# Performance work log

Measured on AMD Instinct MI355X. Metric: run time of the kernel, lower is better.

The kernel has to match this reference:

```python
import jax, jax.numpy as jnp
import numpy as np

H = 2048      # hidden_size
I = 8192      # intermediate_size
NH = 16       # num_heads
HD = H // NH  # head_dim
EPS = 1e-6


def setup_inputs() -> dict:
    key = jax.random.key(0)
    ks = jax.random.split(key, 10)
    s = 0.02
    return {
        "hidden_states": jax.random.normal(ks[0], (2, 2048, H), dtype=jnp.float32),
        "wq": jax.random.normal(ks[1], (H, H), dtype=jnp.float32) * s,
        "wk": jax.random.normal(ks[2], (H, H), dtype=jnp.float32) * s,
        "wv": jax.random.normal(ks[3], (H, H), dtype=jnp.float32) * s,
        "wo": jax.random.normal(ks[4], (H, H), dtype=jnp.float32) * s,
        "w_gate": jax.random.normal(ks[5], (H, I), dtype=jnp.float32) * s,
        "w_up": jax.random.normal(ks[6], (H, I), dtype=jnp.float32) * s,
        "w_down": jax.random.normal(ks[7], (I, H), dtype=jnp.float32) * s,
        "ln1_w": jnp.ones((H,), dtype=jnp.float32),
        "ln2_w": jnp.ones((H,), dtype=jnp.float32),
    }


def rmsnorm(x, w):
    xf = x.astype(jnp.float32)
    var = jnp.mean(xf * xf, axis=-1, keepdims=True)
    return w * (xf * jax.lax.rsqrt(var + EPS)).astype(x.dtype)


def reference(hidden_states, wq, wk, wv, wo, w_gate, w_up, w_down, ln1_w, ln2_w):
    b, s, _ = hidden_states.shape
    residual = hidden_states
    x = rmsnorm(hidden_states, ln1_w)

    # attention (no RoPE, no causal mask, per source)
    q = (x @ wq).reshape(b, s, NH, HD)
    k = (x @ wk).reshape(b, s, NH, HD)
    v = (x @ wv).reshape(b, s, NH, HD)
    scores = jnp.einsum('bqhd,bkhd->bhqk', q, k) / jnp.sqrt(jnp.float32(HD))
    attn = jax.nn.softmax(scores, axis=-1)
    out = jnp.einsum('bhqk,bkhd->bqhd', attn, v).reshape(b, s, H)
    hidden = residual + out @ wo

    residual = hidden
    y = rmsnorm(hidden, ln2_w)
    gate = jax.nn.silu(y @ w_gate)
    up = y @ w_up
    return residual + (gate * up) @ w_down
```

## Files before the change

### kernel.cpp

```cpp
#include <hip/hip_runtime.h>
#include <hip/hip_bf16.h>

#define HDIM 2048
#define IDIM 8192
#define NHEADS 16
#define HEADD 128
#define BATCH 2
#define SEQ 2048
#define MTOK 4096

typedef unsigned short u16;
typedef __bf16 bf16x8 __attribute__((ext_vector_type(8)));
typedef float f32x4 __attribute__((ext_vector_type(4)));
typedef float f32x16 __attribute__((ext_vector_type(16)));
typedef unsigned short u16x8 __attribute__((ext_vector_type(8)));
typedef unsigned int u32x2 __attribute__((ext_vector_type(2)));
typedef unsigned int u32x4 __attribute__((ext_vector_type(4)));
typedef unsigned int uv2 __attribute__((ext_vector_type(2)));

__device__ __forceinline__ u16 f2b(float f) {
  unsigned u = __builtin_bit_cast(unsigned, f);
  u += 0x7FFFu + ((u >> 16) & 1u);
  return (u16)(u >> 16);
}
__device__ __forceinline__ float b2f(u16 b) {
  unsigned u = ((unsigned)b) << 16;
  return __builtin_bit_cast(float, u);
}
__device__ __forceinline__ void gl_lds16(const void* g, void* l) {
  auto gp = (const __attribute__((address_space(1))) unsigned int*)((unsigned long long)g);
  auto lp = (__attribute__((address_space(3))) unsigned int*)((unsigned)(unsigned long long)l);
  __builtin_amdgcn_global_load_lds(gp, lp, 16, 0, 0);
}
__device__ __forceinline__ unsigned cvtpk(float lo, float hi) {
  unsigned r;
  asm("v_cvt_pk_bf16_f32 %0, %1, %2" : "=v"(r) : "v"(lo), "v"(hi));
  return r;
}

__global__ __launch_bounds__(256) void wtrans_all(const float* __restrict__ wq, const float* __restrict__ wk,
                                                  const float* __restrict__ wv, const float* __restrict__ wo,
                                                  const float* __restrict__ wg, const float* __restrict__ wu,
                                                  const float* __restrict__ wd,
                                                  u16* __restrict__ wqkvT, u16* __restrict__ woT,
                                                  u16* __restrict__ wgT, u16* __restrict__ wuT,
                                                  u16* __restrict__ wdT) {
  int bidf = blockIdx.x;
  const float* W;
  u16* Wt;
  int K, N, rowoff, bx, by;
  if (bidf < 3072) {
    int s = bidf >> 10, r = bidf & 1023;
    W = s == 0 ? wq : (s == 1 ? wk : wv);
    Wt = wqkvT; K = 2048; N = 2048; rowoff = s * 2048;
    bx = r & 31; by = r >> 5;
  } else if (bidf < 4096) {
    int r = bidf - 3072;
    W = wo; Wt = woT; K = 2048; N = 2048; rowoff = 0;
    bx = r & 31; by = r >> 5;
  } else if (bidf < 8192) {
    int r = bidf - 4096;
    W = wg; Wt = wgT; K = 2048; N = 8192; rowoff = 0;
    bx = r & 127; by = r >> 7;
  } else if (bidf < 12288) {
    int r = bidf - 8192;
    W = wu; Wt = wuT; K = 2048; N = 8192; rowoff = 0;
    bx = r & 127; by = r >> 7;
  } else {
    int r = bidf - 12288;
    W = wd; Wt = wdT; K = 8192; N = 2048; rowoff = 0;
    bx = r & 31; by = r >> 5;
  }
  __shared__ float t[64][65];
  int n0 = bx * 64, k0 = by * 64;
  int tid = threadIdx.x;
  int kr = tid >> 4, nc = (tid & 15) * 4;
#pragma unroll
  for (int p = 0; p < 4; p++) {
    float4 v = *(const float4*)&W[(size_t)(k0 + p * 16 + kr) * N + n0 + nc];
    t[nc + 0][p * 16 + kr] = v.x;
    t[nc + 1][p * 16 + kr] = v.y;
    t[nc + 2][p * 16 + kr] = v.z;
    t[nc + 3][p * 16 + kr] = v.w;
  }
  __syncthreads();
  int n = tid >> 2, kq = (tid & 3) * 16;
  u16 tmp[16];
#pragma unroll
  for (int i = 0; i < 16; i++) tmp[i] = f2b(t[n][kq + i]);
  *(u16x8*)&Wt[(size_t)(rowoff + n0 + n) * K + k0 + kq] = *(u16x8*)&tmp[0];
  *(u16x8*)&Wt[(size_t)(rowoff + n0 + n) * K + k0 + kq + 8] = *(u16x8*)&tmp[8];
}

__global__ __launch_bounds__(256) void vtrans_k(const u16* __restrict__ qkv, u16* __restrict__ vt) {
  __shared__ u16 t[32][33];
  int s0 = blockIdx.x * 32, d0 = blockIdx.y * 32, bh = blockIdx.z;
  int b = bh >> 4, h = bh & 15;
  int tx = threadIdx.x, ty = threadIdx.y;
#pragma unroll
  for (int i = 0; i < 4; i++)
    t[ty + i * 8][tx] = qkv[(size_t)(b * SEQ + s0 + ty + i * 8) * 6144 + 4096 + h * HEADD + d0 + tx];
  __syncthreads();
#pragma unroll
  for (int i = 0; i < 4; i++)
    vt[(size_t)(bh * HEADD + d0 + ty + i * 8) * SEQ + s0 + tx] = t[tx][ty + i * 8];
}

__global__ __launch_bounds__(256) void rmsnorm_k(const float* __restrict__ X, const float* __restrict__ W,
                                                 u16* __restrict__ O) {
  int row = blockIdx.x;
  int tid = threadIdx.x;
  const float* x = X + (size_t)row * HDIM;
  float4 v0 = ((const float4*)x)[tid * 2];
  float4 v1 = ((const float4*)x)[tid * 2 + 1];
  float ss = v0.x * v0.x + v0.y * v0.y + v0.z * v0.z + v0.w * v0.w
           + v1.x * v1.x + v1.y * v1.y + v1.z * v1.z + v1.w * v1.w;
#pragma unroll
  for (int off = 32; off > 0; off >>= 1) ss += __shfl_down(ss, off);
  __shared__ float red[4];
  if ((tid & 63) == 0) red[tid >> 6] = ss;
  __syncthreads();
  float rs = rsqrtf((red[0] + red[1] + red[2] + red[3]) * (1.0f / HDIM) + 1e-6f);
  const float* w = W + tid * 8;
  u16* o = O + (size_t)row * HDIM + tid * 8;
  float vals[8] = {v0.x, v0.y, v0.z, v0.w, v1.x, v1.y, v1.z, v1.w};
#pragma unroll
  for (int j = 0; j < 8; j++) o[j] = f2b(w[j] * vals[j] * rs);
}

__global__ __launch_bounds__(512, 2) void gemm_fgu(const u16* __restrict__ A, const u16* __restrict__ Bg,
                                                   const u16* __restrict__ Bu, u16* __restrict__ G) {
  __shared__ char lds[131072];
  const int tid = threadIdx.x, lane = tid & 63, w = tid >> 6;
  const int wm = w >> 2, wn = w & 3;
  const int bid = blockIdx.y * 64 + blockIdx.x;
  const int swz = (bid & 7) * 128 + (bid >> 3);
  const int bx = swz & 63, by = swz >> 6;
  const int m0 = by * 256, n0 = bx * 128;
  const int NT = 32;

  const int srow = w * 8 + (lane >> 3);
  const int kko = ((lane & 7) ^ (lane >> 3)) * 8;
  const u16* Asrc = A + (size_t)(m0 + srow) * 2048 + kko;
  const u16* Bgsrc = Bg + (size_t)(n0 + srow) * 2048 + kko;
  const u16* Busrc = Bu + (size_t)(n0 + srow) * 2048 + kko;
  const int wofs = w * 1024;

#define SA0(buf, kt)                                                        \
  {                                                                         \
    gl_lds16(Asrc + (kt) * 64, lds + (buf) * 65536 + wofs);                 \
    gl_lds16(Asrc + 64 * 2048 + (kt) * 64, lds + (buf) * 65536 + 8192 + wofs); \
  }
#define SA1(buf, kt)                                                              \
  {                                                                               \
    gl_lds16(Asrc + 128 * 2048 + (kt) * 64, lds + (buf) * 65536 + 16384 + wofs);  \
    gl_lds16(Asrc + 192 * 2048 + (kt) * 64, lds + (buf) * 65536 + 24576 + wofs);  \
  }
#define SBG(buf, kt)                                                              \
  {                                                                               \
    gl_lds16(Bgsrc + (kt) * 64, lds + (buf) * 65536 + 32768 + wofs);              \
    gl_lds16(Bgsrc + 64 * 2048 + (kt) * 64, lds + (buf) * 65536 + 40960 + wofs);  \
  }
#define SBU(buf, kt)                                                              \
  {                                                                               \
    gl_lds16(Busrc + (kt) * 64, lds + (buf) * 65536 + 49152 + wofs);              \
    gl_lds16(Busrc + 64 * 2048 + (kt) * 64, lds + (buf) * 65536 + 57344 + wofs);  \
  }
#define LG0 { asm volatile("s_waitcnt lgkmcnt(0)" ::: "memory"); __builtin_amdgcn_sched_barrier(0); }

  const int l15 = lane & 15, l4 = lane >> 4;
  const int kq0 = ((l4) ^ (l15 & 7)) << 4;
  const int kq1 = ((4 + l4) ^ (l15 & 7)) << 4;
  const int abase = (wm * 128 + l15) * 128;
  const int gbase = 32768 + (wn * 32 + l15) * 128;
  const int ubase = 49152 + (wn * 32 + l15) * 128;

  const f32x4 fz = {0.f, 0.f, 0.f, 0.f};
  f32x4 ag[8][2], au[8][2];
#pragma unroll
  for (int i = 0; i < 8; i++)
#pragma unroll
    for (int j = 0; j < 2; j++) { ag[i][j] = fz; au[i][j] = fz; }
  bf16x8 af[8], bgf[2], buf2[2];

  SA0(0, 0);
  SBG(0, 0);
  SA1(0, 0);
  SBU(0, 0);
  asm volatile("s_waitcnt vmcnt(2)" ::: "memory");
  __builtin_amdgcn_s_barrier();

  for (int t = 0; t < NT; ++t) {
    const int buf = t & 1, nb = buf ^ 1;
    const char* Lb = lds + buf * 65536;
    const int t1 = (t + 1 < NT) ? t + 1 : NT - 1;
#pragma unroll
    for (int mf = 0; mf < 8; mf++) af[mf] = *(const bf16x8*)(Lb + abase + mf * 2048 + kq0);
    bgf[0] = *(const bf16x8*)(Lb + gbase + kq0);
    bgf[1] = *(const bf16x8*)(Lb + gbase + 2048 + kq0);
    SA0(nb, t1);
    SBG(nb, t1);
    __builtin_amdgcn_s_barrier();
    LG0;
    __builtin_amdgcn_s_setprio(1);
#pragma unroll
    for (int mf = 0; mf < 8; mf++) {
      ag[mf][0] = __builtin_amdgcn_mfma_f32_16x16x32_bf16(af[mf], bgf[0], ag[mf][0], 0, 0, 0);
      ag[mf][1] = __builtin_amdgcn_mfma_f32_16x16x32_bf16(af[mf], bgf[1], ag[mf][1], 0, 0, 0);
    }
    __builtin_amdgcn_s_setprio(0);
    asm volatile("s_waitcnt vmcnt(4)" ::: "memory");
    __builtin_amdgcn_s_barrier();
    buf2[0] = *(const bf16x8*)(Lb + ubase + kq0);
    buf2[1] = *(const bf16x8*)(Lb + ubase + 2048 + kq0);
    SA1(nb, t1);
    __builtin_amdgcn_s_barrier();
    LG0;
    __builtin_amdgcn_s_setprio(1);
#pragma unroll
    for (int mf = 0; mf < 8; mf++) {
      au[mf][0] = __builtin_amdgcn_mfma_f32_16x16x32_bf16(af[mf], buf2[0], au[mf][0], 0, 0, 0);
      au[mf][1] = __builtin_amdgcn_mfma_f32_16x16x32_bf16(af[mf], buf2[1], au[mf][1], 0, 0, 0);
    }
    __builtin_amdgcn_s_setprio(0);
    __builtin_amdgcn_s_barrier();
#pragma unroll
    for (int mf = 0; mf < 8; mf++) af[mf] = *(const bf16x8*)(Lb + abase + mf * 2048 + kq1);
    bgf[0] = *(const bf16x8*)(Lb + gbase + kq1);
    bgf[1] = *(const bf16x8*)(Lb + gbase + 2048 + kq1);
    __builtin_amdgcn_s_barrier();
    LG0;
    __builtin_amdgcn_s_setprio(1);
#pragma unroll
    for (int mf = 0; mf < 8; mf++) {
      ag[mf][0] = __builtin_amdgcn_mfma_f32_16x16x32_bf16(af[mf], bgf[0], ag[mf][0], 0, 0, 0);
      ag[mf][1] = __builtin_amdgcn_mfma_f32_16x16x32_bf16(af[mf], bgf[1], ag[mf][1], 0, 0, 0);
    }
    __builtin_amdgcn_s_setprio(0);
    __builtin_amdgcn_s_barrier();
    buf2[0] = *(const bf16x8*)(Lb + ubase + kq1);
    buf2[1] = *(const bf16x8*)(Lb + ubase + 2048 + kq1);
    SBU(nb, t1);
    __builtin_amdgcn_s_barrier();
    LG0;
    __builtin_amdgcn_s_setprio(1);
#pragma unroll
    for (int mf = 0; mf < 8; mf++) {
      au[mf][0] = __builtin_amdgcn_mfma_f32_16x16x32_bf16(af[mf], buf2[0], au[mf][0], 0, 0, 0);
      au[mf][1] = __builtin_amdgcn_mfma_f32_16x16x32_bf16(af[mf], buf2[1], au[mf][1], 0, 0, 0);
    }
    __builtin_amdgcn_s_setprio(0);
    asm volatile("s_waitcnt vmcnt(2)" ::: "memory");
    __builtin_amdgcn_s_barrier();
  }
  asm volatile("s_waitcnt vmcnt(0)" ::: "memory");

#pragma unroll
  for (int mf = 0; mf < 8; mf++) {
#pragma unroll
    for (int jr = 0; jr < 4; jr++) {
      const int m = m0 + wm * 128 + mf * 16 + l4 * 4 + jr;
#pragma unroll
      for (int nf = 0; nf < 2; nf++) {
        const int n = n0 + wn * 32 + nf * 16 + l15;
        float g = ag[mf][nf][jr];
        float u = au[mf][nf][jr];
        float sg = g / (1.f + __expf(-g));
        G[(size_t)m * IDIM + n] = f2b(sg * u);
      }
    }
  }
#undef SA0
#undef SA1
#undef SBG
#undef SBU
#undef LG0
}

template <int EPI>
__global__ __launch_bounds__(512, 2) void gemm_w(const u16* __restrict__ A, const u16* __restrict__ Bt,
                                                 int M, int N, int K,
                                                 u16* __restrict__ Cb, float* __restrict__ Cf,
                                                 const float* __restrict__ Res, u16* __restrict__ Gm) {
  __shared__ char lds[131072];
  const int tid = threadIdx.x;
  const int lane = tid & 63, w = tid >> 6;
  const int wm = w >> 2, wn = w & 3;
  const int bid = blockIdx.y * gridDim.x + blockIdx.x;
  const int xcd = bid & 7, idx = bid >> 3;
  const int round = idx >> 4, j = idx & 15;
  const int nsy4 = gridDim.y >> 2;
  const int st = round * 8 + xcd;
  const int sx = st / nsy4, syi = st % nsy4;
  const int by = syi * 4 + (j & 3), bx = sx * 4 + (j >> 2);
  const int m0 = by * 256, n0 = bx * 256;
  const int NT = K >> 6;

  const int srow = w * 8 + (lane >> 3);
  const int kko = ((lane & 7) ^ (lane >> 3)) * 8;
  const u16* Asrc = A + (size_t)(m0 + srow) * K + kko;
  const u16* Bsrc = Bt + (size_t)(n0 + srow) * K + kko;
  const int wofs = w * 1024;

#define STAGE_AH(buf, kt, h)                                                          \
  {                                                                                   \
    gl_lds16(Asrc + ((size_t)((h) * 128) * K) + (size_t)(kt) * 64,                    \
             lds + (buf) * 65536 + (h) * 16384 + wofs);                               \
    gl_lds16(Asrc + ((size_t)((h) * 128 + 64) * K) + (size_t)(kt) * 64,               \
             lds + (buf) * 65536 + (h) * 16384 + 8192 + wofs);                        \
  }
#define STAGE_BH(buf, kt, h)                                                          \
  {                                                                                   \
    gl_lds16(Bsrc + ((size_t)((h) * 128) * K) + (size_t)(kt) * 64,                    \
             lds + (buf) * 65536 + 32768 + (h) * 16384 + wofs);                       \
    gl_lds16(Bsrc + ((size_t)((h) * 128 + 64) * K) + (size_t)(kt) * 64,               \
             lds + (buf) * 65536 + 32768 + (h) * 16384 + 8192 + wofs);                \
  }
#define LG0 { asm volatile("s_waitcnt lgkmcnt(0)" ::: "memory"); __builtin_amdgcn_sched_barrier(0); }

  const int l15 = lane & 15, l4 = lane >> 4;
  const int kq0 = ((l4) ^ (l15 & 7)) << 4;
  const int kq1 = ((4 + l4) ^ (l15 & 7)) << 4;
  const int abase = wm * 16384 + l15 * 128;
  const int bbase = 32768 + (wn >> 1) * 16384 + ((wn & 1) * 64 + l15) * 128;

  const f32x4 fz = {0.f, 0.f, 0.f, 0.f};
  f32x4 acc[8][4];
#pragma unroll
  for (int i = 0; i < 8; i++)
#pragma unroll
    for (int jj = 0; jj < 4; jj++) acc[i][jj] = fz;
  bf16x8 af[4], bfr[4];

  STAGE_AH(0, 0, 0);
  STAGE_AH(0, 0, 1);
  STAGE_BH(0, 0, 0);
  STAGE_BH(0, 0, 1);
  STAGE_AH(1, 1, 0);
  STAGE_BH(1, 1, 0);
  asm volatile("s_waitcnt vmcnt(4)" ::: "memory");
  __builtin_amdgcn_s_barrier();

  for (int t = 0; t < NT; ++t) {
    const int buf = t & 1, nbuf = buf ^ 1;
    const char* Lb = lds + buf * 65536;
    const int t1 = (t + 1 < NT) ? t + 1 : NT - 1;
    const int t2 = (t + 2 < NT) ? t + 2 : NT - 1;
#pragma unroll
    for (int mf = 0; mf < 4; mf++) af[mf] = *(const bf16x8*)(Lb + abase + mf * 2048 + kq0);
#pragma unroll
    for (int nf = 0; nf < 4; nf++) bfr[nf] = *(const bf16x8*)(Lb + bbase + nf * 2048 + kq0);
    STAGE_AH(nbuf, t1, 1);
    STAGE_BH(nbuf, t1, 1);
    __builtin_amdgcn_s_barrier();
    LG0;
    __builtin_amdgcn_s_setprio(1);
#pragma unroll
    for (int mf = 0; mf < 4; mf++)
#pragma unroll
      for (int nf = 0; nf < 4; nf++)
        acc[mf][nf] = __builtin_amdgcn_mfma_f32_16x16x32_bf16(af[mf], bfr[nf], acc[mf][nf], 0, 0, 0);
    __builtin_amdgcn_s_setprio(0);
    __builtin_amdgcn_s_barrier();
#pragma unroll
    for (int mf = 0; mf < 4; mf++) af[mf] = *(const bf16x8*)(Lb + abase + (mf + 4) * 2048 + kq0);
    __builtin_amdgcn_s_barrier();
    LG0;
    __builtin_amdgcn_s_setprio(1);
#pragma unroll
    for (int mf = 0; mf < 4; mf++)
#pragma unroll
      for (int nf = 0; nf < 4; nf++)
        acc[mf + 4][nf] = __builtin_amdgcn_mfma_f32_16x16x32_bf16(af[mf], bfr[nf], acc[mf + 4][nf], 0, 0, 0);
    __builtin_amdgcn_s_setprio(0);
    __builtin_amdgcn_s_barrier();
#pragma unroll
    for (int mf = 0; mf < 4; mf++) af[mf] = *(const bf16x8*)(Lb + abase + mf * 2048 + kq1);
#pragma unroll
    for (int nf = 0; nf < 4; nf++) bfr[nf] = *(const bf16x8*)(Lb + bbase + nf * 2048 + kq1);
    __builtin_amdgcn_s_barrier();
    LG0;
    __builtin_amdgcn_s_setprio(1);
#pragma unroll
    for (int mf = 0; mf < 4; mf++)
#pragma unroll
      for (int nf = 0; nf < 4; nf++)
        acc[mf][nf] = __builtin_amdgcn_mfma_f32_16x16x32_bf16(af[mf], bfr[nf], acc[mf][nf], 0, 0, 0);
    __builtin_amdgcn_s_setprio(0);
    __builtin_amdgcn_s_barrier();
#pragma unroll
    for (int mf = 0; mf < 4; mf++) af[mf] = *(const bf16x8*)(Lb + abase + (mf + 4) * 2048 + kq1);
    STAGE_AH(buf, t2, 0);
    STAGE_BH(buf, t2, 0);
    __builtin_amdgcn_s_barrier();
    LG0;
    __builtin_amdgcn_s_setprio(1);
#pragma unroll
    for (int mf = 0; mf < 4; mf++)
#pragma unroll
      for (int nf = 0; nf < 4; nf++)
        acc[mf + 4][nf] = __builtin_amdgcn_mfma_f32_16x16x32_bf16(af[mf], bfr[nf], acc[mf + 4][nf], 0, 0, 0);
    __builtin_amdgcn_s_setprio(0);
    asm volatile("s_waitcnt vmcnt(4)" ::: "memory");
    __builtin_amdgcn_s_barrier();
  }
  asm volatile("s_waitcnt vmcnt(0)" ::: "memory");

  const int r0 = l4 * 4;
#pragma unroll
  for (int mf = 0; mf < 8; mf++) {
#pragma unroll
    for (int jr = 0; jr < 4; jr++) {
      const int m = m0 + wm * 128 + mf * 16 + r0 + jr;
#pragma unroll
      for (int nf = 0; nf < 4; nf++) {
        const int n = n0 + wn * 64 + nf * 16 + l15;
        float v = acc[mf][nf][jr];
        size_t idx = (size_t)m * N + n;
        if (EPI == 0) {
          Cb[idx] = f2b(v);
        } else if (EPI == 3) {
          Cf[idx] = Res[idx] + v;
        }
      }
    }
  }
#undef STAGE_AH
#undef STAGE_BH
#undef LG0
}

template <int EPI>
__global__ __launch_bounds__(512, 2) void gemm256(const u16* __restrict__ A, const u16* __restrict__ Bt,
                                                  int M, int N, int K,
                                                  u16* __restrict__ Cb, float* __restrict__ Cf,
                                                  const float* __restrict__ Res, u16* __restrict__ Gm) {
  __shared__ char lds[98304];
  const int tid = threadIdx.x;
  const int lane = tid & 63, w = tid >> 6;
  const int wm = w >> 1, wn = w & 1;
  const int nwg = gridDim.x * gridDim.y;
  const int bid = blockIdx.y * gridDim.x + blockIdx.x;
  const int swz = (bid & 7) * (nwg >> 3) + (bid >> 3);
  const int bx = swz % gridDim.x, by = swz / gridDim.x;
  const int n0 = bx * 128, m0 = by * 256;
  const int NT = K >> 6;

  const int r8 = lane >> 3, s8 = lane & 7;
  const int slog8 = (s8 ^ r8) * 8;
  const u16* Abase = A + (size_t)(m0 + w * 8 + r8) * K + slog8;
  const u16* Bbase = Bt + (size_t)(n0 + w * 8 + r8) * K + slog8;
  const int stA = w * 1024;

#define STAGE_A(buf, kt, h)                                                        \
  {                                                                                \
    const u16* s_ = Abase + (size_t)(h) * 128 * K + (size_t)(kt) * 64;             \
    gl_lds16(s_, lds + (buf) * 49152 + (h) * 16384 + stA);                         \
    gl_lds16(s_ + 64 * (size_t)K, lds + (buf) * 49152 + (h) * 16384 + stA + 8192); \
  }
#define STAGE_B(buf, kt)                                                     \
  {                                                                          \
    const u16* s_ = Bbase + (size_t)(kt) * 64;                               \
    gl_lds16(s_, lds + (buf) * 49152 + 32768 + stA);                         \
    gl_lds16(s_ + 64 * (size_t)K, lds + (buf) * 49152 + 32768 + stA + 8192); \
  }
#define LG0 { asm volatile("s_waitcnt lgkmcnt(0)" ::: "memory"); __builtin_amdgcn_sched_barrier(0); }

  const int l15 = lane & 15, l4 = lane >> 4;
  const int kq0 = (l4 * 16) ^ ((lane & 7) << 4);
  const int kq1 = (64 + l4 * 16) ^ ((lane & 7) << 4);
  const int aro = (wm >> 1) * 16384 + ((wm & 1) * 64 + l15) * 128;
  const int bro = 32768 + (wn * 64 + l15) * 128;

  const f32x4 fz = {0.f, 0.f, 0.f, 0.f};
  f32x4 acc[4][4];
#pragma unroll
  for (int i = 0; i < 4; i++)
#pragma unroll
    for (int j = 0; j < 4; j++) acc[i][j] = fz;
  bf16x8 af[4][2], bfr[4][2];

  STAGE_A(0, 0, 0);
  STAGE_A(0, 0, 1);
  STAGE_B(0, 0);
  STAGE_A(1, 1, 0);
  STAGE_A(1, 1, 1);
  asm volatile("s_waitcnt vmcnt(4)" ::: "memory");
  __builtin_amdgcn_s_barrier();

  for (int t = 0; t < NT; ++t) {
    const int buf = t & 1;
    const char* Lb = lds + buf * 49152;
    const int t1 = (t + 1 < NT) ? t + 1 : NT - 1;
    const int t2 = (t + 2 < NT) ? t + 2 : NT - 1;
    if (wm < 2) {
#pragma unroll
      for (int mf = 0; mf < 4; mf++) {
        af[mf][0] = *(const bf16x8*)(Lb + aro + mf * 2048 + kq0);
        af[mf][1] = *(const bf16x8*)(Lb + aro + mf * 2048 + kq1);
      }
    } else {
#pragma unroll
      for (int mf = 0; mf < 4; mf++)
        af[mf][0] = *(const bf16x8*)(Lb + aro + mf * 2048 + kq0);
    }
#pragma unroll
    for (int nf = 0; nf < 4; nf++)
      bfr[nf][0] = *(const bf16x8*)(Lb + bro + nf * 2048 + kq0);
    STAGE_B((t + 1) & 1, t1);
    __builtin_amdgcn_s_barrier();
    LG0;
    __builtin_amdgcn_s_setprio(1);
#pragma unroll
    for (int nf = 0; nf < 4; nf++) {
      acc[0][nf] = __builtin_amdgcn_mfma_f32_16x16x32_bf16(af[0][0], bfr[nf][0], acc[0][nf], 0, 0, 0);
      acc[1][nf] = __builtin_amdgcn_mfma_f32_16x16x32_bf16(af[1][0], bfr[nf][0], acc[1][nf], 0, 0, 0);
    }
    __builtin_amdgcn_s_setprio(0);
    __builtin_amdgcn_s_barrier();
    if (wm >= 2) {
#pragma unroll
      for (int mf = 0; mf < 4; mf++)
        af[mf][1] = *(const bf16x8*)(Lb + aro + mf * 2048 + kq1);
    }
#pragma unroll
    for (int nf = 0; nf < 4; nf++)
      bfr[nf][1] = *(const bf16x8*)(Lb + bro + nf * 2048 + kq1);
    STAGE_A(buf, t2, 0);
    __builtin_amdgcn_s_barrier();
    LG0;
    __builtin_amdgcn_s_setprio(1);
#pragma unroll
    for (int nf = 0; nf < 4; nf++) {
      acc[2][nf] = __builtin_amdgcn_mfma_f32_16x16x32_bf16(af[2][0], bfr[nf][0], acc[2][nf], 0, 0, 0);
      acc[3][nf] = __builtin_amdgcn_mfma_f32_16x16x32_bf16(af[3][0], bfr[nf][0], acc[3][nf], 0, 0, 0);
    }
    __builtin_amdgcn_s_setprio(0);
    __builtin_amdgcn_s_barrier();
    STAGE_A(buf, t2, 1);
    __builtin_amdgcn_s_barrier();
    LG0;
    __builtin_amdgcn_s_setprio(1);
#pragma unroll
    for (int nf = 0; nf < 4; nf++) {
      acc[0][nf] = __builtin_amdgcn_mfma_f32_16x16x32_bf16(af[0][1], bfr[nf][1], acc[0][nf], 0, 0, 0);
      acc[1][nf] = __builtin_amdgcn_mfma_f32_16x16x32_bf16(af[1][1], bfr[nf][1], acc[1][nf], 0, 0, 0);
    }
    __builtin_amdgcn_s_setprio(0);
    __builtin_amdgcn_s_barrier();
    __builtin_amdgcn_s_setprio(1);
#pragma unroll
    for (int nf = 0; nf < 4; nf++) {
      acc[2][nf] = __builtin_amdgcn_mfma_f32_16x16x32_bf16(af[2][1], bfr[nf][1], acc[2][nf], 0, 0, 0);
      acc[3][nf] = __builtin_amdgcn_mfma_f32_16x16x32_bf16(af[3][1], bfr[nf][1], acc[3][nf], 0, 0, 0);
    }
    __builtin_amdgcn_s_setprio(0);
    asm volatile("s_waitcnt vmcnt(4)" ::: "memory");
    __builtin_amdgcn_s_barrier();
  }
  asm volatile("s_waitcnt vmcnt(0)" ::: "memory");

  const int r0 = l4 * 4;
#pragma unroll
  for (int mf = 0; mf < 4; mf++) {
#pragma unroll
    for (int j = 0; j < 4; j++) {
      const int m = m0 + wm * 64 + mf * 16 + r0 + j;
#pragma unroll
      for (int nf = 0; nf < 4; nf++) {
        const int n = n0 + wn * 64 + nf * 16 + l15;
        float v = acc[mf][nf][j];
        size_t idx = (size_t)m * N + n;
        if (EPI == 0) {
          Cb[idx] = f2b(v);
        } else if (EPI == 3) {
          Cf[idx] = Res[idx] + v;
        }
      }
    }
  }
#undef STAGE_A
#undef STAGE_B
#undef LG0
}

__global__ __launch_bounds__(512, 2) void attn_k(const u16* __restrict__ qkv, const u16* __restrict__ vt,
                                                 u16* __restrict__ out) {
  __shared__ char Kl[2][16384];
  __shared__ char Vl[2][16384];
  int tid = threadIdx.x, lane = tid & 63, w = tid >> 6;
  int bid = blockIdx.y * 8 + blockIdx.x;
  int swz = (bid & 7) * 32 + (bid >> 3);
  int qb = swz & 7, bh = swz >> 3;
  int b = bh >> 4, h = bh & 15;
  int l31 = lane & 31, hi = lane >> 5;
  const float c = 0.088388347648318447f * 1.4426950408889634f;
  const float RT = 90.51f;

  const int qrow = qb * 256 + w * 32 + l31;
  bf16x8 q[8];
  {
    const u16* qp = qkv + (size_t)(b * SEQ + qrow) * 6144 + h * HEADD + hi * 8;
#pragma unroll
    for (int dt = 0; dt < 8; dt++) q[dt] = *(const bf16x8*)(qp + dt * 16);
  }
  f32x16 o[4];
#pragma unroll
  for (int i = 0; i < 4; i++)
#pragma unroll
    for (int j = 0; j < 16; j++) o[i][j] = 0.f;
  float mrow = -1e30f, lrow = 0.f;

#define ASTAGE(buf, t)                                                                     \
  {                                                                                        \
    int kv0_ = (t) * 64;                                                                   \
    _Pragma("unroll") for (int i = 0; i < 2; i++) {                                        \
      int r = w * 8 + i * 4 + (lane >> 4);                                                 \
      int col = ((lane & 15) ^ (r & 15)) * 8;                                              \
      const u16* src = qkv + (size_t)(b * SEQ + kv0_ + r) * 6144 + HDIM + h * HEADD + col; \
      gl_lds16(src, &Kl[buf][(w * 8 + i * 4) * 256]);                                      \
    }                                                                                      \
    _Pragma("unroll") for (int i = 0; i < 2; i++) {                                        \
      int d = w * 16 + i * 8 + (lane >> 3);                                                \
      int col = ((lane & 7) ^ (d & 7)) * 8;                                                \
      const u16* src = vt + (size_t)(bh * HEADD + d) * SEQ + kv0_ + col;                   \
      gl_lds16(src, &Vl[buf][(w * 16 + i * 8) * 128]);                                     \
    }                                                                                      \
  }

  ASTAGE(0, 0);
  __syncthreads();

  for (int t = 0; t < SEQ / 64; t++) {
    const int buf = t & 1;
    if (t + 1 < SEQ / 64) ASTAGE(buf ^ 1, t + 1);
    const char* Kb = &Kl[buf][0];
    const char* Vb = &Vl[buf][0];
    f32x16 s0, s1;
#pragma unroll
    for (int j = 0; j < 16; j++) { s0[j] = 0.f; s1[j] = 0.f; }
    const int ksl = l31 & 15;
    __builtin_amdgcn_s_setprio(1);
#pragma unroll
    for (int dt = 0; dt < 8; dt++) {
      bf16x8 k0 = *(const bf16x8*)(Kb + (l31)*256 + (((dt * 2 + hi) ^ ksl) << 4));
      bf16x8 k1 = *(const bf16x8*)(Kb + (32 + l31) * 256 + (((dt * 2 + hi) ^ ksl) << 4));
      s0 = __builtin_amdgcn_mfma_f32_32x32x16_bf16(k0, q[dt], s0, 0, 0, 0);
      s1 = __builtin_amdgcn_mfma_f32_32x32x16_bf16(k1, q[dt], s1, 0, 0, 0);
    }
    __builtin_amdgcn_s_setprio(0);
    float m8[8];
#pragma unroll
    for (int g = 0; g < 4; g++) {
      m8[g] = fmaxf(fmaxf(s0[4 * g], s0[4 * g + 1]), fmaxf(s0[4 * g + 2], s0[4 * g + 3]));
      m8[4 + g] = fmaxf(fmaxf(s1[4 * g], s1[4 * g + 1]), fmaxf(s1[4 * g + 2], s1[4 * g + 3]));
    }
    float vmax = fmaxf(fmaxf(fmaxf(m8[0], m8[1]), fmaxf(m8[2], m8[3])),
                       fmaxf(fmaxf(m8[4], m8[5]), fmaxf(m8[6], m8[7])));
    {
      uv2 pr = __builtin_amdgcn_permlane32_swap(__builtin_bit_cast(unsigned, vmax),
                                                __builtin_bit_cast(unsigned, vmax), false, false);
      vmax = fmaxf(__builtin_bit_cast(float, pr[0]), __builtin_bit_cast(float, pr[1]));
    }
    if (__any(vmax > mrow + RT)) {
      float mnew = fmaxf(mrow, vmax);
      float alpha = exp2f((mrow - mnew) * c);
      mrow = mnew;
      lrow *= alpha;
#pragma unroll
      for (int i = 0; i < 4; i++)
#pragma unroll
        for (int j = 0; j < 16; j++) o[i][j] *= alpha;
    }
    const float mc = mrow * c;
    float r4[4] = {0.f, 0.f, 0.f, 0.f};
#pragma unroll
    for (int j = 0; j < 16; j++) {
      s0[j] = exp2f(s0[j] * c - mc);
      r4[j & 3] += s0[j];
    }
#pragma unroll
    for (int j = 0; j < 16; j++) {
      s1[j] = exp2f(s1[j] * c - mc);
      r4[j & 3] += s1[j];
    }
    float rsum = (r4[0] + r4[1]) + (r4[2] + r4[3]);
    {
      uv2 pr = __builtin_amdgcn_permlane32_swap(__builtin_bit_cast(unsigned, rsum),
                                                __builtin_bit_cast(unsigned, rsum), false, false);
      rsum = __builtin_bit_cast(float, pr[0]) + __builtin_bit_cast(float, pr[1]);
    }
    lrow += rsum;
    bf16x8 pa[4];
#pragma unroll
    for (int half = 0; half < 2; half++) {
      const f32x16& sv = half ? s1 : s0;
#pragma unroll
      for (int blk = 0; blk < 2; blk++) {
        int base = blk * 8;
        unsigned A = cvtpk(sv[base + 0], sv[base + 1]);
        unsigned B = cvtpk(sv[base + 2], sv[base + 3]);
        unsigned C = cvtpk(sv[base + 4], sv[base + 5]);
        unsigned D = cvtpk(sv[base + 6], sv[base + 7]);
        uv2 ac = __builtin_amdgcn_permlane32_swap(A, C, false, false);
        uv2 bd = __builtin_amdgcn_permlane32_swap(B, D, false, false);
        u32x4 w4;
        w4[0] = ac[0]; w4[1] = bd[0]; w4[2] = ac[1]; w4[3] = bd[1];
        pa[half * 2 + blk] = __builtin_bit_cast(bf16x8, w4);
      }
    }
    __builtin_amdgcn_s_setprio(1);
#pragma unroll
    for (int dt4 = 0; dt4 < 4; dt4++) {
      const char* vbase = Vb + (dt4 * 32 + l31) * 128;
      const int vsl = l31 & 7;
#pragma unroll
      for (int ks = 0; ks < 4; ks++) {
        bf16x8 vb = *(const bf16x8*)(vbase + (((ks * 2 + hi) ^ vsl) << 4));
        o[dt4] = __builtin_amdgcn_mfma_f32_32x32x16_bf16(vb, pa[ks], o[dt4], 0, 0, 0);
      }
    }
    __builtin_amdgcn_s_setprio(0);
    __syncthreads();
  }
#undef ASTAGE

  const float linv = 1.0f / lrow;
  u16* orow = out + (size_t)(b * SEQ + qrow) * HDIM + h * HEADD;
#pragma unroll
  for (int dt4 = 0; dt4 < 4; dt4++) {
#pragma unroll
    for (int g = 0; g < 4; g++) {
      u32x2 st;
      st[0] = cvtpk(o[dt4][4 * g + 0] * linv, o[dt4][4 * g + 1] * linv);
      st[1] = cvtpk(o[dt4][4 * g + 2] * linv, o[dt4][4 * g + 3] * linv);
      *(u32x2*)(orow + dt4 * 32 + 8 * g + 4 * hi) = st;
    }
  }
}

extern "C" void kernel_launch(void* const* d_in, const int* in_sizes, int n_in,
                              void* d_out, int out_size, void* d_ws, size_t ws_size,
                              hipStream_t stream) {
  const float* hs  = (const float*)d_in[0];
  const float* wq  = (const float*)d_in[1];
  const float* wk  = (const float*)d_in[2];
  const float* wv  = (const float*)d_in[3];
  const float* wo  = (const float*)d_in[4];
  const float* wg  = (const float*)d_in[5];
  const float* wu  = (const float*)d_in[6];
  const float* wd  = (const float*)d_in[7];
  const float* ln1 = (const float*)d_in[8];
  const float* ln2 = (const float*)d_in[9];
  char* ws = (char*)d_ws;
  u16*   wqkvT = (u16*)(ws);
  u16*   woT   = (u16*)(ws + 25165824ull);
  u16*   wgT   = (u16*)(ws + 33554432ull);
  u16*   wuT   = (u16*)(ws + 67108864ull);
  u16*   wdT   = (u16*)(ws + 100663296ull);
  u16*   xb    = (u16*)(ws + 134217728ull);
  float* hid   = (float*)(ws + 150994944ull);
  u16*   qkv   = (u16*)(ws + 184549376ull);
  u16*   vtb   = (u16*)(ws + 234881024ull);
  u16*   attn  = (u16*)(ws + 251658368ull);
  u16*   g     = qkv;

  wtrans_all<<<16384, 256, 0, stream>>>(wq, wk, wv, wo, wg, wu, wd, wqkvT, woT, wgT, wuT, wdT);

  rmsnorm_k<<<MTOK, 256, 0, stream>>>(hs, ln1, xb);
  gemm_w<0><<<dim3(24, 16), 512, 0, stream>>>(xb, wqkvT, MTOK, 6144, HDIM, qkv, nullptr, nullptr, nullptr);
  vtrans_k<<<dim3(64, 4, 32), dim3(32, 8), 0, stream>>>(qkv, vtb);
  attn_k<<<dim3(8, 32), 512, 0, stream>>>(qkv, vtb, attn);
  gemm256<3><<<dim3(16, 16), 512, 0, stream>>>(attn, woT, MTOK, HDIM, HDIM, nullptr, hid, hs, nullptr);
  rmsnorm_k<<<MTOK, 256, 0, stream>>>(hid, ln2, xb);
  gemm_fgu<<<dim3(64, 16), 512, 0, stream>>>(xb, wgT, wuT, g);
  gemm256<3><<<dim3(16, 16), 512, 0, stream>>>(g, wdT, MTOK, HDIM, IDIM, nullptr, (float*)d_out, hid, nullptr);
}
```

Before: 726.7 us.

## Unify GEMMs into 256x128-tile kernel with rectangular XCD-aware block swizzle

Replaces the 256x256 QKV GEMM and the 256x128 gemm256 kernel with a single new gemm_s kernel. It uses 256x128 tiles, 8x2 MFMA fragments per wave, and a simpler two-phase double-buffered schedule. The QKV launch grid doubles to 48x16 blocks. A rectangular 4x8 block-group swizzle spread across XCDs is applied to gemm_s and gemm_fgu for L2 locality. Smaller tiles raise block count and occupancy for QKV but lower per-block data reuse, and the new schedule has fewer barriers but coarser overlap.

```diff
diff --git a/kernel.cpp b/kernel.cpp
--- a/kernel.cpp
+++ b/kernel.cpp
@@ -128,14 +128,133 @@
   for (int j = 0; j < 8; j++) o[j] = f2b(w[j] * vals[j] * rs);
 }
 
+template <int EPI>
+__global__ __launch_bounds__(512, 2) void gemm_s(const u16* __restrict__ A, const u16* __restrict__ Bt,
+                                                 int M, int N, int K,
+                                                 u16* __restrict__ Cb, float* __restrict__ Cf,
+                                                 const float* __restrict__ Res) {
+  __shared__ char lds[98304];
+  const int tid = threadIdx.x, lane = tid & 63, w = tid >> 6;
+  const int wm = w >> 2, wn = w & 3;
+  const int GX = gridDim.x;
+  const int bid = blockIdx.y * GX + blockIdx.x;
+  const int xcd = bid & 7, ii = bid >> 3;
+  const int j = ii & 31, rin = ii >> 5;
+  const int rectIdx = rin * 8 + xcd;
+  const int nry = gridDim.y >> 2;
+  const int ry = rectIdx % nry, rx = rectIdx / nry;
+  const int by = ry * 4 + (j >> 3), bx = rx * 8 + (j & 7);
+  const int m0 = by * 256, n0 = bx * 128;
+  const int NT = K >> 6;
+
+  const int srow = w * 8 + (lane >> 3);
+  const int kko = ((lane & 7) ^ (lane >> 3)) * 8;
+  const u16* Asrc = A + (size_t)(m0 + srow) * K + kko;
+  const u16* Bsrc = Bt + (size_t)(n0 + srow) * K + kko;
+  const int wofs = w * 1024;
+
+#define SSA(buf, kt)                                                                  \
+  {                                                                                   \
+    gl_lds16(Asrc + (size_t)(kt) * 64, lds + (buf) * 49152 + wofs);                   \
+    gl_lds16(Asrc + 64 * (size_t)K + (size_t)(kt) * 64, lds + (buf) * 49152 + 8192 + wofs);   \
+    gl_lds16(Asrc + 128 * (size_t)K + (size_t)(kt) * 64, lds + (buf) * 49152 + 16384 + wofs); \
+    gl_lds16(Asrc + 192 * (size_t)K + (size_t)(kt) * 64, lds + (buf) * 49152 + 24576 + wofs); \
+  }
+#define SSB(buf, kt)                                                                  \
+  {                                                                                   \
+    gl_lds16(Bsrc + (size_t)(kt) * 64, lds + (buf) * 49152 + 32768 + wofs);           \
+    gl_lds16(Bsrc + 64 * (size_t)K + (size_t)(kt) * 64, lds + (buf) * 49152 + 40960 + wofs);  \
+  }
+
+  const int l15 = lane & 15, l4 = lane >> 4;
+  const int kq0 = ((l4) ^ (l15 & 7)) << 4;
+  const int kq1 = ((4 + l4) ^ (l15 & 7)) << 4;
+  const int abase = wm * 16384 + l15 * 128;
+  const int bbase = 32768 + (wn * 32 + l15) * 128;
+
+  const f32x4 fz = {0.f, 0.f, 0.f, 0.f};
+  f32x4 acc[8][2];
+#pragma unroll
+  for (int i = 0; i < 8; i++) { acc[i][0] = fz; acc[i][1] = fz; }
+  bf16x8 af[8], bq0[2], bq1[2];
+
+  SSA(0, 0);
+  SSB(0, 0);
+  asm volatile("s_waitcnt vmcnt(2)" ::: "memory");
+  __builtin_amdgcn_s_barrier();
+
+  for (int t = 0; t < NT; ++t) {
+    const int buf = t & 1, nb = buf ^ 1;
+    const char* Lb = lds + buf * 49152;
+    const int t1 = (t + 1 < NT) ? t + 1 : NT - 1;
+#pragma unroll
+    for (int mf = 0; mf < 8; mf++) af[mf] = *(const bf16x8*)(Lb + abase + mf * 2048 + kq0);
+    SSA(nb, t1);
+    asm volatile("s_waitcnt vmcnt(4)" ::: "memory");
+    __builtin_amdgcn_s_barrier();
+    bq0[0] = *(const bf16x8*)(Lb + bbase + kq0);
+    bq0[1] = *(const bf16x8*)(Lb + bbase + 2048 + kq0);
+    bq1[0] = *(const bf16x8*)(Lb + bbase + kq1);
+    bq1[1] = *(const bf16x8*)(Lb + bbase + 2048 + kq1);
+    asm volatile("s_waitcnt lgkmcnt(0)" ::: "memory");
+    __builtin_amdgcn_sched_barrier(0);
+    __builtin_amdgcn_s_setprio(1);
+#pragma unroll
+    for (int mf = 0; mf < 8; mf++) {
+      acc[mf][0] = __builtin_amdgcn_mfma_f32_16x16x32_bf16(af[mf], bq0[0], acc[mf][0], 0, 0, 0);
+      acc[mf][1] = __builtin_amdgcn_mfma_f32_16x16x32_bf16(af[mf], bq0[1], acc[mf][1], 0, 0, 0);
+    }
+    __builtin_amdgcn_s_setprio(0);
+#pragma unroll
+    for (int mf = 0; mf < 8; mf++) af[mf] = *(const bf16x8*)(Lb + abase + mf * 2048 + kq1);
+    SSB(nb, t1);
+    asm volatile("s_waitcnt vmcnt(2)" ::: "memory");
+    asm volatile("s_waitcnt lgkmcnt(0)" ::: "memory");
+    __builtin_amdgcn_sched_barrier(0);
+    __builtin_amdgcn_s_barrier();
+    __builtin_amdgcn_s_setprio(1);
+#pragma unroll
+    for (int mf = 0; mf < 8; mf++) {
+      acc[mf][0] = __builtin_amdgcn_mfma_f32_16x16x32_bf16(af[mf], bq1[0], acc[mf][0], 0, 0, 0);
+      acc[mf][1] = __builtin_amdgcn_mfma_f32_16x16x32_bf16(af[mf], bq1[1], acc[mf][1], 0, 0, 0);
+    }
+    __builtin_amdgcn_s_setprio(0);
+  }
+  asm volatile("s_waitcnt vmcnt(0)" ::: "memory");
+
+#pragma unroll
+  for (int mf = 0; mf < 8; mf++) {
+#pragma unroll
+    for (int jr = 0; jr < 4; jr++) {
+      const int m = m0 + wm * 128 + mf * 16 + l4 * 4 + jr;
+#pragma unroll
+      for (int nf = 0; nf < 2; nf++) {
+        const int n = n0 + wn * 32 + nf * 16 + l15;
+        float v = acc[mf][nf][jr];
+        size_t idx = (size_t)m * N + n;
+        if (EPI == 0) {
+          Cb[idx] = f2b(v);
+        } else {
+          Cf[idx] = Res[idx] + v;
+        }
+      }
+    }
+  }
+#undef SSA
+#undef SSB
+}
+
 __global__ __launch_bounds__(512, 2) void gemm_fgu(const u16* __restrict__ A, const u16* __restrict__ Bg,
                                                    const u16* __restrict__ Bu, u16* __restrict__ G) {
   __shared__ char lds[131072];
   const int tid = threadIdx.x, lane = tid & 63, w = tid >> 6;
   const int wm = w >> 2, wn = w & 3;
   const int bid = blockIdx.y * 64 + blockIdx.x;
-  const int swz = (bid & 7) * 128 + (bid >> 3);
-  const int bx = swz & 63, by = swz >> 6;
+  const int xcd = bid & 7, ii = bid >> 3;
+  const int j = ii & 31, rin = ii >> 5;
+  const int rectIdx = rin * 8 + xcd;
+  const int ry = rectIdx & 3, rx = rectIdx >> 2;
+  const int by = ry * 4 + (j >> 3), bx = rx * 8 + (j & 7);
   const int m0 = by * 256, n0 = bx * 128;
   const int NT = 32;
 
@@ -180,7 +299,7 @@
 #pragma unroll
   for (int i = 0; i < 8; i++)
 #pragma unroll
-    for (int j = 0; j < 2; j++) { ag[i][j] = fz; au[i][j] = fz; }
+    for (int jj = 0; jj < 2; jj++) { ag[i][jj] = fz; au[i][jj] = fz; }
   bf16x8 af[8], bgf[2], buf2[2];
 
   SA0(0, 0);
@@ -274,313 +393,6 @@
 #undef SA1
 #undef SBG
 #undef SBU
-#undef LG0
-}
-
-template <int EPI>
-__global__ __launch_bounds__(512, 2) void gemm_w(const u16* __restrict__ A, const u16* __restrict__ Bt,
-                                                 int M, int N, int K,
-                                                 u16* __restrict__ Cb, float* __restrict__ Cf,
-                                                 const float* __restrict__ Res, u16* __restrict__ Gm) {
-  __shared__ char lds[131072];
-  const int tid = threadIdx.x;
-  const int lane = tid & 63, w = tid >> 6;
-  const int wm = w >> 2, wn = w & 3;
-  const int bid = blockIdx.y * gridDim.x + blockIdx.x;
-  const int xcd = bid & 7, idx = bid >> 3;
-  const int round = idx >> 4, j = idx & 15;
-  const int nsy4 = gridDim.y >> 2;
-  const int st = round * 8 + xcd;
-  const int sx = st / nsy4, syi = st % nsy4;
-  const int by = syi * 4 + (j & 3), bx = sx * 4 + (j >> 2);
-  const int m0 = by * 256, n0 = bx * 256;
-  const int NT = K >> 6;
-
-  const int srow = w * 8 + (lane >> 3);
-  const int kko = ((lane & 7) ^ (lane >> 3)) * 8;
-  const u16* Asrc = A + (size_t)(m0 + srow) * K + kko;
-  const u16* Bsrc = Bt + (size_t)(n0 + srow) * K + kko;
-  const int wofs = w * 1024;
-
-#define STAGE_AH(buf, kt, h)                                                          \
-  {                                                                                   \
-    gl_lds16(Asrc + ((size_t)((h) * 128) * K) + (size_t)(kt) * 64,                    \
-             lds + (buf) * 65536 + (h) * 16384 + wofs);                               \
-    gl_lds16(Asrc + ((size_t)((h) * 128 + 64) * K) + (size_t)(kt) * 64,               \
-             lds + (buf) * 65536 + (h) * 16384 + 8192 + wofs);                        \
-  }
-#define STAGE_BH(buf, kt, h)                                                          \
-  {                                                                                   \
-    gl_lds16(Bsrc + ((size_t)((h) * 128) * K) + (size_t)(kt) * 64,                    \
-             lds + (buf) * 65536 + 32768 + (h) * 16384 + wofs);                       \
-    gl_lds16(Bsrc + ((size_t)((h) * 128 + 64) * K) + (size_t)(kt) * 64,               \
-             lds + (buf) * 65536 + 32768 + (h) * 16384 + 8192 + wofs);                \
-  }
-#define LG0 { asm volatile("s_waitcnt lgkmcnt(0)" ::: "memory"); __builtin_amdgcn_sched_barrier(0); }
-
-  const int l15 = lane & 15, l4 = lane >> 4;
-  const int kq0 = ((l4) ^ (l15 & 7)) << 4;
-  const int kq1 = ((4 + l4) ^ (l15 & 7)) << 4;
-  const int abase = wm * 16384 + l15 * 128;
-  const int bbase = 32768 + (wn >> 1) * 16384 + ((wn & 1) * 64 + l15) * 128;
-
-  const f32x4 fz = {0.f, 0.f, 0.f, 0.f};
-  f32x4 acc[8][4];
-#pragma unroll
-  for (int i = 0; i < 8; i++)
-#pragma unroll
-    for (int jj = 0; jj < 4; jj++) acc[i][jj] = fz;
-  bf16x8 af[4], bfr[4];
-
-  STAGE_AH(0, 0, 0);
-  STAGE_AH(0, 0, 1);
-  STAGE_BH(0, 0, 0);
-  STAGE_BH(0, 0, 1);
-  STAGE_AH(1, 1, 0);
-  STAGE_BH(1, 1, 0);
-  asm volatile("s_waitcnt vmcnt(4)" ::: "memory");
-  __builtin_amdgcn_s_barrier();
-
-  for (int t = 0; t < NT; ++t) {
-    const int buf = t & 1, nbuf = buf ^ 1;
-    const char* Lb = lds + buf * 65536;
-    const int t1 = (t + 1 < NT) ? t + 1 : NT - 1;
-    const int t2 = (t + 2 < NT) ? t + 2 : NT - 1;
-#pragma unroll
-    for (int mf = 0; mf < 4; mf++) af[mf] = *(const bf16x8*)(Lb + abase + mf * 2048 + kq0);
-#pragma unroll
-    for (int nf = 0; nf < 4; nf++) bfr[nf] = *(const bf16x8*)(Lb + bbase + nf * 2048 + kq0);
-    STAGE_AH(nbuf, t1, 1);
-    STAGE_BH(nbuf, t1, 1);
-    __builtin_amdgcn_s_barrier();
-    LG0;
-    __builtin_amdgcn_s_setprio(1);
-#pragma unroll
-    for (int mf = 0; mf < 4; mf++)
-#pragma unroll
-      for (int nf = 0; nf < 4; nf++)
-        acc[mf][nf] = __builtin_amdgcn_mfma_f32_16x16x32_bf16(af[mf], bfr[nf], acc[mf][nf], 0, 0, 0);
-    __builtin_amdgcn_s_setprio(0);
-    __builtin_amdgcn_s_barrier();
-#pragma unroll
-    for (int mf = 0; mf < 4; mf++) af[mf] = *(const bf16x8*)(Lb + abase + (mf + 4) * 2048 + kq0);
-    __builtin_amdgcn_s_barrier();
-    LG0;
-    __builtin_amdgcn_s_setprio(1);
-#pragma unroll
-    for (int mf = 0; mf < 4; mf++)
-#pragma unroll
-      for (int nf = 0; nf < 4; nf++)
-        acc[mf + 4][nf] = __builtin_amdgcn_mfma_f32_16x16x32_bf16(af[mf], bfr[nf], acc[mf + 4][nf], 0, 0, 0);
-    __builtin_amdgcn_s_setprio(0);
-    __builtin_amdgcn_s_barrier();
-#pragma unroll
-    for (int mf = 0; mf < 4; mf++) af[mf] = *(const bf16x8*)(Lb + abase + mf * 2048 + kq1);
-#pragma unroll
-    for (int nf = 0; nf < 4; nf++) bfr[nf] = *(const bf16x8*)(Lb + bbase + nf * 2048 + kq1);
-    __builtin_amdgcn_s_barrier();
-    LG0;
-    __builtin_amdgcn_s_setprio(1);
-#pragma unroll
-    for (int mf = 0; mf < 4; mf++)
-#pragma unroll
-      for (int nf = 0; nf < 4; nf++)
-        acc[mf][nf] = __builtin_amdgcn_mfma_f32_16x16x32_bf16(af[mf], bfr[nf], acc[mf][nf], 0, 0, 0);
-    __builtin_amdgcn_s_setprio(0);
-    __builtin_amdgcn_s_barrier();
-#pragma unroll
-    for (int mf = 0; mf < 4; mf++) af[mf] = *(const bf16x8*)(Lb + abase + (mf + 4) * 2048 + kq1);
-    STAGE_AH(buf, t2, 0);
-    STAGE_BH(buf, t2, 0);
-    __builtin_amdgcn_s_barrier();
-    LG0;
-    __builtin_amdgcn_s_setprio(1);
-#pragma unroll
-    for (int mf = 0; mf < 4; mf++)
-#pragma unroll
-      for (int nf = 0; nf < 4; nf++)
-        acc[mf + 4][nf] = __builtin_amdgcn_mfma_f32_16x16x32_bf16(af[mf], bfr[nf], acc[mf + 4][nf], 0, 0, 0);
-    __builtin_amdgcn_s_setprio(0);
-    asm volatile("s_waitcnt vmcnt(4)" ::: "memory");
-    __builtin_amdgcn_s_barrier();
-  }
-  asm volatile("s_waitcnt vmcnt(0)" ::: "memory");
-
-  const int r0 = l4 * 4;
-#pragma unroll
-  for (int mf = 0; mf < 8; mf++) {
-#pragma unroll
-    for (int jr = 0; jr < 4; jr++) {
-      const int m = m0 + wm * 128 + mf * 16 + r0 + jr;
-#pragma unroll
-      for (int nf = 0; nf < 4; nf++) {
-        const int n = n0 + wn * 64 + nf * 16 + l15;
-        float v = acc[mf][nf][jr];
-        size_t idx = (size_t)m * N + n;
-        if (EPI == 0) {
-          Cb[idx] = f2b(v);
-        } else if (EPI == 3) {
-          Cf[idx] = Res[idx] + v;
-        }
-      }
-    }
-  }
-#undef STAGE_AH
-#undef STAGE_BH
-#undef LG0
-}
-
-template <int EPI>
-__global__ __launch_bounds__(512, 2) void gemm256(const u16* __restrict__ A, const u16* __restrict__ Bt,
-                                                  int M, int N, int K,
-                                                  u16* __restrict__ Cb, float* __restrict__ Cf,
-                                                  const float* __restrict__ Res, u16* __restrict__ Gm) {
-  __shared__ char lds[98304];
-  const int tid = threadIdx.x;
-  const int lane = tid & 63, w = tid >> 6;
-  const int wm = w >> 1, wn = w & 1;
-  const int nwg = gridDim.x * gridDim.y;
-  const int bid = blockIdx.y * gridDim.x + blockIdx.x;
-  const int swz = (bid & 7) * (nwg >> 3) + (bid >> 3);
-  const int bx = swz % gridDim.x, by = swz / gridDim.x;
-  const int n0 = bx * 128, m0 = by * 256;
-  const int NT = K >> 6;
-
-  const int r8 = lane >> 3, s8 = lane & 7;
-  const int slog8 = (s8 ^ r8) * 8;
-  const u16* Abase = A + (size_t)(m0 + w * 8 + r8) * K + slog8;
-  const u16* Bbase = Bt + (size_t)(n0 + w * 8 + r8) * K + slog8;
-  const int stA = w * 1024;
-
-#define STAGE_A(buf, kt, h)                                                        \
-  {                                                                                \
-    const u16* s_ = Abase + (size_t)(h) * 128 * K + (size_t)(kt) * 64;             \
-    gl_lds16(s_, lds + (buf) * 49152 + (h) * 16384 + stA);                         \
-    gl_lds16(s_ + 64 * (size_t)K, lds + (buf) * 49152 + (h) * 16384 + stA + 8192); \
-  }
-#define STAGE_B(buf, kt)                                                     \
-  {                                                                          \
-    const u16* s_ = Bbase + (size_t)(kt) * 64;                               \
-    gl_lds16(s_, lds + (buf) * 49152 + 32768 + stA);                         \
-    gl_lds16(s_ + 64 * (size_t)K, lds + (buf) * 49152 + 32768 + stA + 8192); \
-  }
-#define LG0 { asm volatile("s_waitcnt lgkmcnt(0)" ::: "memory"); __builtin_amdgcn_sched_barrier(0); }
-
-  const int l15 = lane & 15, l4 = lane >> 4;
-  const int kq0 = (l4 * 16) ^ ((lane & 7) << 4);
-  const int kq1 = (64 + l4 * 16) ^ ((lane & 7) << 4);
-  const int aro = (wm >> 1) * 16384 + ((wm & 1) * 64 + l15) * 128;
-  const int bro = 32768 + (wn * 64 + l15) * 128;
-
-  const f32x4 fz = {0.f, 0.f, 0.f, 0.f};
-  f32x4 acc[4][4];
-#pragma unroll
-  for (int i = 0; i < 4; i++)
-#pragma unroll
-    for (int j = 0; j < 4; j++) acc[i][j] = fz;
-  bf16x8 af[4][2], bfr[4][2];
-
-  STAGE_A(0, 0, 0);
-  STAGE_A(0, 0, 1);
-  STAGE_B(0, 0);
-  STAGE_A(1, 1, 0);
-  STAGE_A(1, 1, 1);
-  asm volatile("s_waitcnt vmcnt(4)" ::: "memory");
-  __builtin_amdgcn_s_barrier();
-
-  for (int t = 0; t < NT; ++t) {
-    const int buf = t & 1;
-    const char* Lb = lds + buf * 49152;
-    const int t1 = (t + 1 < NT) ? t + 1 : NT - 1;
-    const int t2 = (t + 2 < NT) ? t + 2 : NT - 1;
-    if (wm < 2) {
-#pragma unroll
-      for (int mf = 0; mf < 4; mf++) {
-        af[mf][0] = *(const bf16x8*)(Lb + aro + mf * 2048 + kq0);
-        af[mf][1] = *(const bf16x8*)(Lb + aro + mf * 2048 + kq1);
-      }
-    } else {
-#pragma unroll
-      for (int mf = 0; mf < 4; mf++)
-        af[mf][0] = *(const bf16x8*)(Lb + aro + mf * 2048 + kq0);
-    }
-#pragma unroll
-    for (int nf = 0; nf < 4; nf++)
-      bfr[nf][0] = *(const bf16x8*)(Lb + bro + nf * 2048 + kq0);
-    STAGE_B((t + 1) & 1, t1);
-    __builtin_amdgcn_s_barrier();
-    LG0;
-    __builtin_amdgcn_s_setprio(1);
-#pragma unroll
-    for (int nf = 0; nf < 4; nf++) {
-      acc[0][nf] = __builtin_amdgcn_mfma_f32_16x16x32_bf16(af[0][0], bfr[nf][0], acc[0][nf], 0, 0, 0);
-      acc[1][nf] = __builtin_amdgcn_mfma_f32_16x16x32_bf16(af[1][0], bfr[nf][0], acc[1][nf], 0, 0, 0);
-    }
-    __builtin_amdgcn_s_setprio(0);
-    __builtin_amdgcn_s_barrier();
-    if (wm >= 2) {
-#pragma unroll
-      for (int mf = 0; mf < 4; mf++)
-        af[mf][1] = *(const bf16x8*)(Lb + aro + mf * 2048 + kq1);
-    }
-#pragma unroll
-    for (int nf = 0; nf < 4; nf++)
-      bfr[nf][1] = *(const bf16x8*)(Lb + bro + nf * 2048 + kq1);
-    STAGE_A(buf, t2, 0);
-    __builtin_amdgcn_s_barrier();
-    LG0;
-    __builtin_amdgcn_s_setprio(1);
-#pragma unroll
-    for (int nf = 0; nf < 4; nf++) {
-      acc[2][nf] = __builtin_amdgcn_mfma_f32_16x16x32_bf16(af[2][0], bfr[nf][0], acc[2][nf], 0, 0, 0);
-      acc[3][nf] = __builtin_amdgcn_mfma_f32_16x16x32_bf16(af[3][0], bfr[nf][0], acc[3][nf], 0, 0, 0);
-    }
-    __builtin_amdgcn_s_setprio(0);
-    __builtin_amdgcn_s_barrier();
-    STAGE_A(buf, t2, 1);
-    __builtin_amdgcn_s_barrier();
-    LG0;
-    __builtin_amdgcn_s_setprio(1);
-#pragma unroll
-    for (int nf = 0; nf < 4; nf++) {
-      acc[0][nf] = __builtin_amdgcn_mfma_f32_16x16x32_bf16(af[0][1], bfr[nf][1], acc[0][nf], 0, 0, 0);
-      acc[1][nf] = __builtin_amdgcn_mfma_f32_16x16x32_bf16(af[1][1], bfr[nf][1], acc[1][nf], 0, 0, 0);
-    }
-    __builtin_amdgcn_s_setprio(0);
-    __builtin_amdgcn_s_barrier();
-    __builtin_amdgcn_s_setprio(1);
-#pragma unroll
-    for (int nf = 0; nf < 4; nf++) {
-      acc[2][nf] = __builtin_amdgcn_mfma_f32_16x16x32_bf16(af[2][1], bfr[nf][1], acc[2][nf], 0, 0, 0);
-      acc[3][nf] = __builtin_amdgcn_mfma_f32_16x16x32_bf16(af[3][1], bfr[nf][1], acc[3][nf], 0, 0, 0);
-    }
-    __builtin_amdgcn_s_setprio(0);
-    asm volatile("s_waitcnt vmcnt(4)" ::: "memory");
-    __builtin_amdgcn_s_barrier();
-  }
-  asm volatile("s_waitcnt vmcnt(0)" ::: "memory");
-
-  const int r0 = l4 * 4;
-#pragma unroll
-  for (int mf = 0; mf < 4; mf++) {
-#pragma unroll
-    for (int j = 0; j < 4; j++) {
-      const int m = m0 + wm * 64 + mf * 16 + r0 + j;
-#pragma unroll
-      for (int nf = 0; nf < 4; nf++) {
-        const int n = n0 + wn * 64 + nf * 16 + l15;
-        float v = acc[mf][nf][j];
-        size_t idx = (size_t)m * N + n;
-        if (EPI == 0) {
-          Cb[idx] = f2b(v);
-        } else if (EPI == 3) {
-          Cf[idx] = Res[idx] + v;
-        }
-      }
-    }
-  }
-#undef STAGE_A
-#undef STAGE_B
 #undef LG0
 }
 
@@ -768,11 +580,11 @@
   wtrans_all<<<16384, 256, 0, stream>>>(wq, wk, wv, wo, wg, wu, wd, wqkvT, woT, wgT, wuT, wdT);
 
   rmsnorm_k<<<MTOK, 256, 0, stream>>>(hs, ln1, xb);
-  gemm_w<0><<<dim3(24, 16), 512, 0, stream>>>(xb, wqkvT, MTOK, 6144, HDIM, qkv, nullptr, nullptr, nullptr);
+  gemm_s<0><<<dim3(48, 16), 512, 0, stream>>>(xb, wqkvT, MTOK, 6144, HDIM, qkv, nullptr, nullptr);
   vtrans_k<<<dim3(64, 4, 32), dim3(32, 8), 0, stream>>>(qkv, vtb);
   attn_k<<<dim3(8, 32), 512, 0, stream>>>(qkv, vtb, attn);
-  gemm256<3><<<dim3(16, 16), 512, 0, stream>>>(attn, woT, MTOK, HDIM, HDIM, nullptr, hid, hs, nullptr);
+  gemm_s<3><<<dim3(16, 16), 512, 0, stream>>>(attn, woT, MTOK, HDIM, HDIM, nullptr, hid, hs);
   rmsnorm_k<<<MTOK, 256, 0, stream>>>(hid, ln2, xb);
   gemm_fgu<<<dim3(64, 16), 512, 0, stream>>>(xb, wgT, wuT, g);
-  gemm256<3><<<dim3(16, 16), 512, 0, stream>>>(g, wdT, MTOK, HDIM, IDIM, nullptr, (float*)d_out, hid, nullptr);
-}
+  gemm_s<3><<<dim3(16, 16), 512, 0, stream>>>(g, wdT, MTOK, HDIM, IDIM, nullptr, (float*)d_out, hid);
+}
```

Result: no change. 723.7 us (-0.4%).
